# Kernel optimization log

Hardware: AMD Instinct MI355X
Metric: run time of the kernel (lower is better)

## Reference

```python
import jax, jax.numpy as jnp
import numpy as np

N_NODES = 100000


def gcn_layer(x, edge_index, W, b):
    """PyG GCNConv: h = D^-1/2 (A+I) D^-1/2 (x W) + b, scatter-sum aggregation."""
    n = x.shape[0]
    h = x @ W  # [N, out]
    loop = jnp.arange(n, dtype=edge_index.dtype)
    src = jnp.concatenate([edge_index[0], loop])  # [E+N]
    dst = jnp.concatenate([edge_index[1], loop])
    deg = jax.ops.segment_sum(jnp.ones_like(dst, dtype=h.dtype), dst, num_segments=n)
    dinv = jnp.where(deg > 0, jax.lax.rsqrt(deg), 0.0)
    norm = dinv[src] * dinv[dst]  # [E+N]
    msg = h[src] * norm[:, None]  # gather + scale (largest intermediate)
    out = jax.ops.segment_sum(msg, dst, num_segments=n)
    return out + b


def setup_inputs() -> dict:
    key = jax.random.key(0)
    k = jax.random.split(key, 8)
    in_dim, hid_dim, out_dim = 128, 64, 112
    E = 1600000
    x = jax.random.normal(k[0], (N_NODES, in_dim), dtype=jnp.float32)
    edge_index = jax.random.randint(k[1], (2, E), 0, N_NODES, dtype=jnp.int32)
    s1 = 1.0 / np.sqrt(in_dim)
    s2 = 1.0 / np.sqrt(hid_dim)
    return {
        "x": x,
        "edge_index": edge_index,
        "W1": jax.random.uniform(k[2], (in_dim, hid_dim), jnp.float32, -s1, s1),
        "b1": jnp.zeros((hid_dim,), jnp.float32),
        "W2": jax.random.uniform(k[3], (hid_dim, hid_dim), jnp.float32, -s2, s2),
        "b2": jnp.zeros((hid_dim,), jnp.float32),
        "W3": jax.random.uniform(k[4], (hid_dim, out_dim), jnp.float32, -s2, s2),
        "b3": jnp.zeros((out_dim,), jnp.float32),
    }


def reference(x, edge_index, W1, b1, W2, b2, W3, b3):
    # eval mode: dropout is identity
    h = jax.nn.relu(gcn_layer(x, edge_index, W1, b1))
    h = jax.nn.relu(gcn_layer(h, edge_index, W2, b2))
    return gcn_layer(h, edge_index, W3, b3)
```

## Files before the change

### kernel.cpp

```cpp
#include <hip/hip_runtime.h>
#include <hip/hip_fp16.h>
#include <math.h>


#define IN_DIM 128
#define HID 64
#define OUT_DIM 112
#define SCAN_TILE 1024
#define LSHIFT 7
#define LMASK 127
#define MAXBUCK 1024
#define CHUNK 4096
#define CAP 4096

typedef _Float16 f16x8 __attribute__((ext_vector_type(8)));
typedef float f32x4 __attribute__((ext_vector_type(4)));

template <int K, int C, bool XH, bool DINV, bool BIAS, bool OUTH>
__device__ __forceinline__ void mfma_gemm_tile(int blk, const void* __restrict__ Xv,
                                               const float* __restrict__ W,
                                               const float* __restrict__ dinv,
                                               const float* __restrict__ bias,
                                               void* __restrict__ G, int n,
                                               _Float16* Wt) {
  constexpr int KP = K + 8;
  constexpr int NT = C / 16;
  constexpr int KS = K / 32;
  const int tid = threadIdx.x;
  for (int idx = tid; idx < K * C; idx += 256) {
    int k = idx / C, c = idx % C;
    Wt[c * KP + k] = (_Float16)W[idx];
  }
  __syncthreads();

  const int wv = tid >> 6, l = tid & 63;
  const int rbase = blk * 64 + wv * 16;
  const int kg = (l >> 4) * 8;
  const int c16 = l & 15;

  int arow = rbase + c16;
  if (arow >= n) arow = n - 1;
  f16x8 af[KS];
  if (XH) {
    const _Float16* Xh = reinterpret_cast<const _Float16*>(Xv);
#pragma unroll
    for (int ks = 0; ks < KS; ++ks)
      af[ks] = *reinterpret_cast<const f16x8*>(&Xh[(size_t)arow * K + ks * 32 + kg]);
  } else {
    const float* Xf = reinterpret_cast<const float*>(Xv);
#pragma unroll
    for (int ks = 0; ks < KS; ++ks) {
      float4 u0 = *reinterpret_cast<const float4*>(&Xf[(size_t)arow * K + ks * 32 + kg]);
      float4 u1 = *reinterpret_cast<const float4*>(&Xf[(size_t)arow * K + ks * 32 + kg + 4]);
      f16x8 a;
      a[0] = (_Float16)u0.x; a[1] = (_Float16)u0.y; a[2] = (_Float16)u0.z; a[3] = (_Float16)u0.w;
      a[4] = (_Float16)u1.x; a[5] = (_Float16)u1.y; a[6] = (_Float16)u1.z; a[7] = (_Float16)u1.w;
      af[ks] = a;
    }
  }

  f32x4 acc[NT];
#pragma unroll
  for (int nt = 0; nt < NT; ++nt) acc[nt] = (f32x4){0.f, 0.f, 0.f, 0.f};

#pragma unroll
  for (int ks = 0; ks < KS; ++ks) {
#pragma unroll
    for (int nt = 0; nt < NT; ++nt) {
      f16x8 bf = *reinterpret_cast<const f16x8*>(&Wt[(nt * 16 + c16) * KP + ks * 32 + kg]);
      acc[nt] = __builtin_amdgcn_mfma_f32_16x16x32_f16(af[ks], bf, acc[nt], 0, 0, 0);
    }
  }

#pragma unroll
  for (int r = 0; r < 4; ++r) {
    int grow = rbase + (l >> 4) * 4 + r;
    if (grow < n) {
      float s = DINV ? dinv[grow] : 1.0f;
#pragma unroll
      for (int nt = 0; nt < NT; ++nt) {
        float v = acc[nt][r] * s;
        if (BIAS) v += bias[nt * 16 + c16];
        if (OUTH)
          reinterpret_cast<__half*>(G)[(size_t)grow * C + nt * 16 + c16] = __float2half(v);
        else
          reinterpret_cast<float*>(G)[(size_t)grow * C + nt * 16 + c16] = v;
      }
    }
  }
}

template <int K, int C, bool XH, bool DINV, bool BIAS, bool OUTH>
__global__ __launch_bounds__(256) void mfma_gemm_kernel(const void* __restrict__ Xv,
                                                        const float* __restrict__ W,
                                                        const float* __restrict__ dinv,
                                                        const float* __restrict__ bias,
                                                        void* __restrict__ G, int n) {
  __shared__ _Float16 Wt[C * (K + 8)];
  mfma_gemm_tile<K, C, XH, DINV, BIAS, OUTH>(blockIdx.x, Xv, W, dinv, bias, G, n, Wt);
}

__global__ __launch_bounds__(256) void gemm1_scatter_kernel(
    const float* __restrict__ x, const float* __restrict__ W1, __half* __restrict__ gh,
    int n, const int* __restrict__ src, const int* __restrict__ dst,
    int* __restrict__ cur0, int* __restrict__ packed, int E, int nbuck, int nchunk) {
  __shared__ _Float16 Wt[HID * (IN_DIM + 8)];
  __shared__ int hist[MAXBUCK];
  __shared__ int cur[MAXBUCK];
  const int tid = threadIdx.x;
  if ((int)blockIdx.x < nchunk) {
    for (int i = tid; i < nbuck; i += 256) hist[i] = 0;
    __syncthreads();
    const int lo = blockIdx.x * CHUNK;
    const int hi = min(E, lo + CHUNK);
    for (int i = lo + tid; i < hi; i += 256)
      atomicAdd(&hist[dst[i] >> LSHIFT], 1);
    __syncthreads();
    for (int b = tid; b < nbuck; b += 256) {
      int c = hist[b];
      cur[b] = (c > 0) ? atomicAdd(&cur0[b], c) : 0;
    }
    __syncthreads();
    for (int i = lo + tid; i < hi; i += 256) {
      int s = src[i], d = dst[i];
      int b = d >> LSHIFT;
      int off = atomicAdd(&cur[b], 1);
      if (off < CAP) packed[b * CAP + off] = (s << LSHIFT) | (d & LMASK);
    }
  } else {
    mfma_gemm_tile<IN_DIM, HID, false, false, false, true>(
        (int)blockIdx.x - nchunk, x, W1, nullptr, nullptr, gh, n, Wt);
  }
}

__global__ __launch_bounds__(256) void fine_count_kernel(const int* __restrict__ packed,
                                                         const int* __restrict__ cur0,
                                                         int* __restrict__ cnt,
                                                         float* __restrict__ dinv, int n) {
  int b = blockIdx.x;
  __shared__ int hist[128];
  int t = threadIdx.x;
  if (t < 128) hist[t] = 0;
  __syncthreads();
  int cb = min(cur0[b], CAP);
  const int* pk = &packed[b * CAP];
  for (int e = t; e < cb; e += 256) atomicAdd(&hist[pk[e] & LMASK], 1);
  __syncthreads();
  int node = b * 128 + t;
  if (t < 128 && node < n) {
    cnt[node] = hist[t];
    dinv[node] = 1.0f / sqrtf((float)(hist[t] + 1));
  }
}

__global__ __launch_bounds__(256) void fine_scatter_kernel(const int* __restrict__ packed,
                                                           const int* __restrict__ cur0,
                                                           const int* __restrict__ row_start,
                                                           int* __restrict__ ssrc, int n) {
  int b = blockIdx.x;
  __shared__ int cur[128];
  int t = threadIdx.x;
  if (t < 128) {
    int node = b * 128 + t;
    cur[t] = (node < n) ? row_start[node] : 0;
  }
  __syncthreads();
  int cb = min(cur0[b], CAP);
  const int* pk = &packed[b * CAP];
  for (int e = t; e < cb; e += 256) {
    int p = pk[e];
    int slot = atomicAdd(&cur[p & LMASK], 1);
    ssrc[slot] = p >> LSHIFT;
  }
}


__global__ __launch_bounds__(256) void scan_partial_kernel(const int* __restrict__ cnt,
                                                           int* __restrict__ blocksum,
                                                           int n) {
  int t = threadIdx.x;
  int base = blockIdx.x * SCAN_TILE + t * 4;
  int s = 0;
  if (base + 4 <= n) {
    int4 v = *reinterpret_cast<const int4*>(&cnt[base]);
    s = v.x + v.y + v.z + v.w;
  } else {
    for (int i = 0; i < 4; ++i)
      if (base + i < n) s += cnt[base + i];
  }
#pragma unroll
  for (int off = 1; off < 64; off <<= 1) s += __shfl_xor(s, off);
  __shared__ int wsum[4];
  int lane = t & 63, wv = t >> 6;
  if (lane == 0) wsum[wv] = s;
  __syncthreads();
  if (t == 0) blocksum[blockIdx.x] = wsum[0] + wsum[1] + wsum[2] + wsum[3];
}

__global__ __launch_bounds__(1024) void scan_blocksums_kernel(int* __restrict__ blocksum,
                                                              int* __restrict__ total_out,
                                                              int nb) {
  __shared__ int sh[1024];
  int t = threadIdx.x;
  int v = (t < nb) ? blocksum[t] : 0;
  sh[t] = v;
  __syncthreads();
  for (int off = 1; off < 1024; off <<= 1) {
    int u = (t >= off) ? sh[t - off] : 0;
    __syncthreads();
    sh[t] += u;
    __syncthreads();
  }
  if (t < nb) blocksum[t] = sh[t] - v;
  if (t == 1023) *total_out = sh[1023];
}

__global__ __launch_bounds__(256) void scan_final_kernel(const int* __restrict__ cnt,
                                                         const int* __restrict__ blocksum,
                                                         int* __restrict__ row_start, int n) {
  int t = threadIdx.x;
  int base = blockIdx.x * SCAN_TILE + t * 4;
  int v0 = 0, v1 = 0, v2 = 0, v3 = 0;
  if (base + 4 <= n) {
    int4 v = *reinterpret_cast<const int4*>(&cnt[base]);
    v0 = v.x; v1 = v.y; v2 = v.z; v3 = v.w;
  } else {
    if (base + 0 < n) v0 = cnt[base + 0];
    if (base + 1 < n) v1 = cnt[base + 1];
    if (base + 2 < n) v2 = cnt[base + 2];
    if (base + 3 < n) v3 = cnt[base + 3];
  }
  int s = v0 + v1 + v2 + v3;
  __shared__ int sh[256];
  sh[t] = s;
  __syncthreads();
  for (int off = 1; off < 256; off <<= 1) {
    int u = (t >= off) ? sh[t - off] : 0;
    __syncthreads();
    sh[t] += u;
    __syncthreads();
  }
  int run = blocksum[blockIdx.x] + sh[t] - s;
  int p0 = run, p1 = run + v0, p2 = p1 + v1, p3 = p2 + v2;
  if (base + 4 <= n) {
    *reinterpret_cast<int4*>(&row_start[base]) = make_int4(p0, p1, p2, p3);
  } else {
    if (base + 0 < n) row_start[base + 0] = p0;
    if (base + 1 < n) row_start[base + 1] = p1;
    if (base + 2 < n) row_start[base + 2] = p2;
    if (base + 3 < n) row_start[base + 3] = p3;
  }
}

template <int C, bool RELU, bool BIAS, bool TSCALE, bool OUTH, bool SRCSCALE>
__global__ __launch_bounds__(256) void agg_kernel(const __half* __restrict__ g,
                                                  const int* __restrict__ row_start,
                                                  const int* __restrict__ ssrc,
                                                  const float* __restrict__ dinv,
                                                  const float* __restrict__ bias,
                                                  void* __restrict__ out, int n) {
  static_assert(C == 64, "agg assumes 64 channels");
  const int tid = threadIdx.x;
  const int wv = tid >> 6;
  const int lane = tid & 63;
  const int h = lane >> 5;
  const int q = lane & 31;
  int node = blockIdx.x * 4 + wv;
  if (node >= n) return;
  const __half2* g2 = reinterpret_cast<const __half2*>(g);

  int e0 = row_start[node];
  int e1 = row_start[node + 1];
  int deg = e1 - e0;
  float di = dinv[node];
  float2 acc = make_float2(0.f, 0.f);
  if (h == 0) {
    float2 sv = __half22float2(g2[(size_t)node * 32 + q]);
    float w = SRCSCALE ? di : 1.0f;
    acc.x = sv.x * w; acc.y = sv.y * w;
  }
  const int pairs = deg >> 1;
  const int base = e0 + h;
  int k = 0;
  for (; k + 8 <= pairs; k += 8) {
    int idx[8];
#pragma unroll
    for (int i = 0; i < 8; ++i) idx[i] = ssrc[base + 2 * (k + i)];
    __half2 v[8];
#pragma unroll
    for (int i = 0; i < 8; ++i) v[i] = g2[(size_t)idx[i] * 32 + q];
    float ds[8];
    if (SRCSCALE) {
#pragma unroll
      for (int i = 0; i < 8; ++i) ds[i] = dinv[idx[i]];
    }
#pragma unroll
    for (int i = 0; i < 8; ++i) {
      float2 f = __half22float2(v[i]);
      if (SRCSCALE) {
        acc.x = fmaf(f.x, ds[i], acc.x); acc.y = fmaf(f.y, ds[i], acc.y);
      } else {
        acc.x += f.x; acc.y += f.y;
      }
    }
  }
  for (; k < pairs; ++k) {
    int i0 = ssrc[base + 2 * k];
    float2 f = __half22float2(g2[(size_t)i0 * 32 + q]);
    float w = SRCSCALE ? dinv[i0] : 1.0f;
    acc.x = fmaf(f.x, w, acc.x); acc.y = fmaf(f.y, w, acc.y);
  }
  if ((deg & 1) && h == 0) {
    int i0 = ssrc[e1 - 1];
    float2 f = __half22float2(g2[(size_t)i0 * 32 + q]);
    float w = SRCSCALE ? dinv[i0] : 1.0f;
    acc.x = fmaf(f.x, w, acc.x); acc.y = fmaf(f.y, w, acc.y);
  }
  acc.x += __shfl_xor(acc.x, 32);
  acc.y += __shfl_xor(acc.y, 32);

  if (h == 0) {
    float rx = acc.x * di, ry = acc.y * di;
    if (BIAS) {
      float2 bv = *reinterpret_cast<const float2*>(&bias[2 * q]);
      rx += bv.x; ry += bv.y;
    }
    if (RELU) { rx = fmaxf(rx, 0.f); ry = fmaxf(ry, 0.f); }
    if (TSCALE) { rx *= di; ry *= di; }
    if (OUTH) {
      reinterpret_cast<__half2*>(out)[(size_t)node * 32 + q] = __floats2half2_rn(rx, ry);
    } else {
      reinterpret_cast<float2*>(out)[(size_t)node * 32 + q] = make_float2(rx, ry);
    }
  }
}

extern "C" void kernel_launch(void* const* d_in, const int* in_sizes, int n_in,
                              void* d_out, int out_size, void* d_ws, size_t ws_size,
                              hipStream_t stream) {
  const float* x = (const float*)d_in[0];
  const int* ei = (const int*)d_in[1];
  const float* W1 = (const float*)d_in[2];
  const float* b1 = (const float*)d_in[3];
  const float* W2 = (const float*)d_in[4];
  const float* b2 = (const float*)d_in[5];
  const float* W3 = (const float*)d_in[6];
  const float* b3 = (const float*)d_in[7];
  float* out = (float*)d_out;

  const int n = in_sizes[0] / IN_DIM;
  const int E = in_sizes[1] / 2;
  const int* src = ei;
  const int* dst = ei + E;
  const int nbuck = (n + LMASK) >> LSHIFT;
  const int nchunk = (E + CHUNK - 1) / CHUNK;

  char* p = (char*)d_ws;
  auto alloc = [&](size_t bytes) {
    char* q = p;
    p += (bytes + 255) & ~(size_t)255;
    return q;
  };
  float* dinv = (float*)alloc((size_t)n * 4);
  int* row_start = (int*)alloc((size_t)(n + 1) * 4);
  int* cnt = (int*)alloc((size_t)n * 4);
  int* blocksum = (int*)alloc((size_t)1024 * 4);
  int* cur0 = (int*)alloc((size_t)MAXBUCK * 4);
  int* packed = (int*)alloc((size_t)nbuck * CAP * 4);
  int* ssrc = (int*)alloc((size_t)E * 4);
  __half* gh  = (__half*)alloc((size_t)n * HID * 2);
  __half* h1h = (__half*)alloc((size_t)n * HID * 2);
  __half* th  = (__half*)alloc((size_t)n * HID * 2);
  __half* zh  = h1h;

  const int NB = (n + SCAN_TILE - 1) / SCAN_TILE;
  const int GGRID = (n + 63) / 64;

  hipMemsetAsync(cur0, 0, (size_t)nbuck * 4, stream);
  gemm1_scatter_kernel<<<nchunk + GGRID, 256, 0, stream>>>(x, W1, gh, n, src, dst,
                                                           cur0, packed, E, nbuck, nchunk);
  fine_count_kernel<<<nbuck, 256, 0, stream>>>(packed, cur0, cnt, dinv, n);
  scan_partial_kernel<<<NB, 256, 0, stream>>>(cnt, blocksum, n);
  scan_blocksums_kernel<<<1, 1024, 0, stream>>>(blocksum, &row_start[n], NB);
  scan_final_kernel<<<NB, 256, 0, stream>>>(cnt, blocksum, row_start, n);
  fine_scatter_kernel<<<nbuck, 256, 0, stream>>>(packed, cur0, row_start, ssrc, n);

  agg_kernel<HID, true, true, false, true, true><<<(n + 3) / 4, 256, 0, stream>>>(gh, row_start, ssrc, dinv, b1, h1h, n);

  mfma_gemm_kernel<HID, HID, true, true, false, true><<<GGRID, 256, 0, stream>>>(h1h, W2, dinv, nullptr, gh, n);
  agg_kernel<HID, true, true, true, true, false><<<(n + 3) / 4, 256, 0, stream>>>(gh, row_start, ssrc, dinv, b2, th, n);

  agg_kernel<HID, false, false, false, true, false><<<(n + 3) / 4, 256, 0, stream>>>(th, row_start, ssrc, dinv, nullptr, zh, n);
  mfma_gemm_kernel<HID, OUT_DIM, true, false, true, false><<<GGRID, 256, 0, stream>>>(zh, W3, nullptr, b3, out, n);
}
```

Baseline: 384.7 us.

## Fuse fine count, scan, scatter and source prescale into one CSR kernel

Replaces the fine count, three-kernel scan and fine scatter with one per-bucket kernel. Each bucket computes its row offset by summing the coarse bucket counts that precede it, then runs an in-block prefix over its 128 nodes. The same kernel also prescales the layer-1 features by dinv, so the first aggregation no longer gathers dinv for every edge. It additionally merges shared-memory buffers in the first kernel and adds a two-pair unrolled tail loop in aggregation. The cost is a redundant O(nbuck) prefix read per block and an extra read-modify-write pass over the layer-1 feature buffer.

```diff
diff --git a/kernel.cpp b/kernel.cpp
--- a/kernel.cpp
+++ b/kernel.cpp
@@ -6,7 +6,6 @@
 #define IN_DIM 128
 #define HID 64
 #define OUT_DIM 112
-#define SCAN_TILE 1024
 #define LSHIFT 7
 #define LMASK 127
 #define MAXBUCK 1024
@@ -104,11 +103,11 @@
     const float* __restrict__ x, const float* __restrict__ W1, __half* __restrict__ gh,
     int n, const int* __restrict__ src, const int* __restrict__ dst,
     int* __restrict__ cur0, int* __restrict__ packed, int E, int nbuck, int nchunk) {
-  __shared__ _Float16 Wt[HID * (IN_DIM + 8)];
-  __shared__ int hist[MAXBUCK];
-  __shared__ int cur[MAXBUCK];
+  __shared__ __align__(16) char smem[HID * (IN_DIM + 8) * 2];
   const int tid = threadIdx.x;
   if ((int)blockIdx.x < nchunk) {
+    int* hist = reinterpret_cast<int*>(smem);
+    int* cur = hist + MAXBUCK;
     for (int i = tid; i < nbuck; i += 256) hist[i] = 0;
     __syncthreads();
     const int lo = blockIdx.x * CHUNK;
@@ -128,131 +127,80 @@
       if (off < CAP) packed[b * CAP + off] = (s << LSHIFT) | (d & LMASK);
     }
   } else {
+    _Float16* Wt = reinterpret_cast<_Float16*>(smem);
     mfma_gemm_tile<IN_DIM, HID, false, false, false, true>(
         (int)blockIdx.x - nchunk, x, W1, nullptr, nullptr, gh, n, Wt);
   }
 }
 
-__global__ __launch_bounds__(256) void fine_count_kernel(const int* __restrict__ packed,
-                                                         const int* __restrict__ cur0,
-                                                         int* __restrict__ cnt,
-                                                         float* __restrict__ dinv, int n) {
-  int b = blockIdx.x;
+__global__ __launch_bounds__(256) void fine_fused_kernel(
+    const int* __restrict__ packed, const int* __restrict__ cur0,
+    int* __restrict__ row_start, float* __restrict__ dinv,
+    int* __restrict__ ssrc, __half* __restrict__ gh, int n, int nbuck) {
+  const int b = blockIdx.x;
+  const int t = threadIdx.x;
   __shared__ int hist[128];
-  int t = threadIdx.x;
+  __shared__ int pfx[128];
+  __shared__ int cur[128];
+  __shared__ float sdi[128];
+  __shared__ int red[4];
+  __shared__ int sbase;
   if (t < 128) hist[t] = 0;
   __syncthreads();
-  int cb = min(cur0[b], CAP);
-  const int* pk = &packed[b * CAP];
+  const int cb = min(cur0[b], CAP);
+  const int* pk = &packed[(size_t)b * CAP];
   for (int e = t; e < cb; e += 256) atomicAdd(&hist[pk[e] & LMASK], 1);
-  __syncthreads();
-  int node = b * 128 + t;
-  if (t < 128 && node < n) {
-    cnt[node] = hist[t];
-    dinv[node] = 1.0f / sqrtf((float)(hist[t] + 1));
-  }
-}
-
-__global__ __launch_bounds__(256) void fine_scatter_kernel(const int* __restrict__ packed,
-                                                           const int* __restrict__ cur0,
-                                                           const int* __restrict__ row_start,
-                                                           int* __restrict__ ssrc, int n) {
-  int b = blockIdx.x;
-  __shared__ int cur[128];
-  int t = threadIdx.x;
+  int partial = 0;
+  for (int i = t; i < b; i += 256) partial += min(cur0[i], CAP);
+#pragma unroll
+  for (int off = 1; off < 64; off <<= 1) partial += __shfl_xor(partial, off);
+  const int lane = t & 63, wv = t >> 6;
+  if (lane == 0) red[wv] = partial;
+  __syncthreads();
+  if (t == 0) sbase = red[0] + red[1] + red[2] + red[3];
+  if (t < 128) pfx[t] = hist[t];
+  __syncthreads();
+  for (int off = 1; off < 128; off <<= 1) {
+    int u = (t >= off && t < 128) ? pfx[t - off] : 0;
+    __syncthreads();
+    if (t < 128) pfx[t] += u;
+    __syncthreads();
+  }
   if (t < 128) {
     int node = b * 128 + t;
-    cur[t] = (node < n) ? row_start[node] : 0;
-  }
-  __syncthreads();
-  int cb = min(cur0[b], CAP);
-  const int* pk = &packed[b * CAP];
+    if (node < n) {
+      int rs = sbase + pfx[t] - hist[t];
+      row_start[node] = rs;
+      float di = 1.0f / sqrtf((float)(hist[t] + 1));
+      dinv[node] = di;
+      sdi[t] = di;
+      cur[t] = rs;
+    } else {
+      sdi[t] = 0.f;
+      cur[t] = 0;
+    }
+  }
+  if (b == nbuck - 1 && t == 0) row_start[n] = sbase + cb;
+  __syncthreads();
   for (int e = t; e < cb; e += 256) {
     int p = pk[e];
     int slot = atomicAdd(&cur[p & LMASK], 1);
     ssrc[slot] = p >> LSHIFT;
   }
-}
-
-
-__global__ __launch_bounds__(256) void scan_partial_kernel(const int* __restrict__ cnt,
-                                                           int* __restrict__ blocksum,
-                                                           int n) {
-  int t = threadIdx.x;
-  int base = blockIdx.x * SCAN_TILE + t * 4;
-  int s = 0;
-  if (base + 4 <= n) {
-    int4 v = *reinterpret_cast<const int4*>(&cnt[base]);
-    s = v.x + v.y + v.z + v.w;
-  } else {
-    for (int i = 0; i < 4; ++i)
-      if (base + i < n) s += cnt[base + i];
-  }
-#pragma unroll
-  for (int off = 1; off < 64; off <<= 1) s += __shfl_xor(s, off);
-  __shared__ int wsum[4];
-  int lane = t & 63, wv = t >> 6;
-  if (lane == 0) wsum[wv] = s;
-  __syncthreads();
-  if (t == 0) blocksum[blockIdx.x] = wsum[0] + wsum[1] + wsum[2] + wsum[3];
-}
-
-__global__ __launch_bounds__(1024) void scan_blocksums_kernel(int* __restrict__ blocksum,
-                                                              int* __restrict__ total_out,
-                                                              int nb) {
-  __shared__ int sh[1024];
-  int t = threadIdx.x;
-  int v = (t < nb) ? blocksum[t] : 0;
-  sh[t] = v;
-  __syncthreads();
-  for (int off = 1; off < 1024; off <<= 1) {
-    int u = (t >= off) ? sh[t - off] : 0;
-    __syncthreads();
-    sh[t] += u;
-    __syncthreads();
-  }
-  if (t < nb) blocksum[t] = sh[t] - v;
-  if (t == 1023) *total_out = sh[1023];
-}
-
-__global__ __launch_bounds__(256) void scan_final_kernel(const int* __restrict__ cnt,
-                                                         const int* __restrict__ blocksum,
-                                                         int* __restrict__ row_start, int n) {
-  int t = threadIdx.x;
-  int base = blockIdx.x * SCAN_TILE + t * 4;
-  int v0 = 0, v1 = 0, v2 = 0, v3 = 0;
-  if (base + 4 <= n) {
-    int4 v = *reinterpret_cast<const int4*>(&cnt[base]);
-    v0 = v.x; v1 = v.y; v2 = v.z; v3 = v.w;
-  } else {
-    if (base + 0 < n) v0 = cnt[base + 0];
-    if (base + 1 < n) v1 = cnt[base + 1];
-    if (base + 2 < n) v2 = cnt[base + 2];
-    if (base + 3 < n) v3 = cnt[base + 3];
-  }
-  int s = v0 + v1 + v2 + v3;
-  __shared__ int sh[256];
-  sh[t] = s;
-  __syncthreads();
-  for (int off = 1; off < 256; off <<= 1) {
-    int u = (t >= off) ? sh[t - off] : 0;
-    __syncthreads();
-    sh[t] += u;
-    __syncthreads();
-  }
-  int run = blocksum[blockIdx.x] + sh[t] - s;
-  int p0 = run, p1 = run + v0, p2 = p1 + v1, p3 = p2 + v2;
-  if (base + 4 <= n) {
-    *reinterpret_cast<int4*>(&row_start[base]) = make_int4(p0, p1, p2, p3);
-  } else {
-    if (base + 0 < n) row_start[base + 0] = p0;
-    if (base + 1 < n) row_start[base + 1] = p1;
-    if (base + 2 < n) row_start[base + 2] = p2;
-    if (base + 3 < n) row_start[base + 3] = p3;
-  }
-}
-
-template <int C, bool RELU, bool BIAS, bool TSCALE, bool OUTH, bool SRCSCALE>
+  __half2* g2 = reinterpret_cast<__half2*>(gh);
+  for (int i = t; i < 128 * 32; i += 256) {
+    int nd = i >> 5;
+    int node = b * 128 + nd;
+    if (node < n) {
+      int q = i & 31;
+      float2 f = __half22float2(g2[(size_t)node * 32 + q]);
+      float d = sdi[nd];
+      g2[(size_t)node * 32 + q] = __floats2half2_rn(f.x * d, f.y * d);
+    }
+  }
+}
+
+template <int C, bool RELU, bool BIAS, bool TSCALE, bool OUTH>
 __global__ __launch_bounds__(256) void agg_kernel(const __half* __restrict__ g,
                                                   const int* __restrict__ row_start,
                                                   const int* __restrict__ ssrc,
@@ -272,12 +220,10 @@
   int e0 = row_start[node];
   int e1 = row_start[node + 1];
   int deg = e1 - e0;
-  float di = dinv[node];
   float2 acc = make_float2(0.f, 0.f);
   if (h == 0) {
     float2 sv = __half22float2(g2[(size_t)node * 32 + q]);
-    float w = SRCSCALE ? di : 1.0f;
-    acc.x = sv.x * w; acc.y = sv.y * w;
+    acc.x = sv.x; acc.y = sv.y;
   }
   const int pairs = deg >> 1;
   const int base = e0 + h;
@@ -289,37 +235,34 @@
     __half2 v[8];
 #pragma unroll
     for (int i = 0; i < 8; ++i) v[i] = g2[(size_t)idx[i] * 32 + q];
-    float ds[8];
-    if (SRCSCALE) {
-#pragma unroll
-      for (int i = 0; i < 8; ++i) ds[i] = dinv[idx[i]];
-    }
 #pragma unroll
     for (int i = 0; i < 8; ++i) {
       float2 f = __half22float2(v[i]);
-      if (SRCSCALE) {
-        acc.x = fmaf(f.x, ds[i], acc.x); acc.y = fmaf(f.y, ds[i], acc.y);
-      } else {
-        acc.x += f.x; acc.y += f.y;
-      }
-    }
+      acc.x += f.x; acc.y += f.y;
+    }
+  }
+  for (; k + 2 <= pairs; k += 2) {
+    int i0 = ssrc[base + 2 * k];
+    int i1 = ssrc[base + 2 * (k + 1)];
+    float2 f0 = __half22float2(g2[(size_t)i0 * 32 + q]);
+    float2 f1 = __half22float2(g2[(size_t)i1 * 32 + q]);
+    acc.x += f0.x + f1.x; acc.y += f0.y + f1.y;
   }
   for (; k < pairs; ++k) {
     int i0 = ssrc[base + 2 * k];
     float2 f = __half22float2(g2[(size_t)i0 * 32 + q]);
-    float w = SRCSCALE ? dinv[i0] : 1.0f;
-    acc.x = fmaf(f.x, w, acc.x); acc.y = fmaf(f.y, w, acc.y);
+    acc.x += f.x; acc.y += f.y;
   }
   if ((deg & 1) && h == 0) {
     int i0 = ssrc[e1 - 1];
     float2 f = __half22float2(g2[(size_t)i0 * 32 + q]);
-    float w = SRCSCALE ? dinv[i0] : 1.0f;
-    acc.x = fmaf(f.x, w, acc.x); acc.y = fmaf(f.y, w, acc.y);
+    acc.x += f.x; acc.y += f.y;
   }
   acc.x += __shfl_xor(acc.x, 32);
   acc.y += __shfl_xor(acc.y, 32);
 
   if (h == 0) {
+    float di = dinv[node];
     float rx = acc.x * di, ry = acc.y * di;
     if (BIAS) {
       float2 bv = *reinterpret_cast<const float2*>(&bias[2 * q]);
@@ -363,8 +306,6 @@
   };
   float* dinv = (float*)alloc((size_t)n * 4);
   int* row_start = (int*)alloc((size_t)(n + 1) * 4);
-  int* cnt = (int*)alloc((size_t)n * 4);
-  int* blocksum = (int*)alloc((size_t)1024 * 4);
   int* cur0 = (int*)alloc((size_t)MAXBUCK * 4);
   int* packed = (int*)alloc((size_t)nbuck * CAP * 4);
   int* ssrc = (int*)alloc((size_t)E * 4);
@@ -373,23 +314,18 @@
   __half* th  = (__half*)alloc((size_t)n * HID * 2);
   __half* zh  = h1h;
 
-  const int NB = (n + SCAN_TILE - 1) / SCAN_TILE;
   const int GGRID = (n + 63) / 64;
 
-  hipMemsetAsync(cur0, 0, (size_t)nbuck * 4, stream);
+  hipMemsetAsync(cur0, 0, (size_t)MAXBUCK * 4, stream);
   gemm1_scatter_kernel<<<nchunk + GGRID, 256, 0, stream>>>(x, W1, gh, n, src, dst,
                                                            cur0, packed, E, nbuck, nchunk);
-  fine_count_kernel<<<nbuck, 256, 0, stream>>>(packed, cur0, cnt, dinv, n);
-  scan_partial_kernel<<<NB, 256, 0, stream>>>(cnt, blocksum, n);
-  scan_blocksums_kernel<<<1, 1024, 0, stream>>>(blocksum, &row_start[n], NB);
-  scan_final_kernel<<<NB, 256, 0, stream>>>(cnt, blocksum, row_start, n);
-  fine_scatter_kernel<<<nbuck, 256, 0, stream>>>(packed, cur0, row_start, ssrc, n);
-
-  agg_kernel<HID, true, true, false, true, true><<<(n + 3) / 4, 256, 0, stream>>>(gh, row_start, ssrc, dinv, b1, h1h, n);
+  fine_fused_kernel<<<nbuck, 256, 0, stream>>>(packed, cur0, row_start, dinv, ssrc, gh, n, nbuck);
+
+  agg_kernel<HID, true, true, false, true><<<(n + 3) / 4, 256, 0, stream>>>(gh, row_start, ssrc, dinv, b1, h1h, n);
 
   mfma_gemm_kernel<HID, HID, true, true, false, true><<<GGRID, 256, 0, stream>>>(h1h, W2, dinv, nullptr, gh, n);
-  agg_kernel<HID, true, true, true, true, false><<<(n + 3) / 4, 256, 0, stream>>>(gh, row_start, ssrc, dinv, b2, th, n);
-
-  agg_kernel<HID, false, false, false, true, false><<<(n + 3) / 4, 256, 0, stream>>>(th, row_start, ssrc, dinv, nullptr, zh, n);
+  agg_kernel<HID, true, true, true, true><<<(n + 3) / 4, 256, 0, stream>>>(gh, row_start, ssrc, dinv, b2, th, n);
+
+  agg_kernel<HID, false, false, false, true><<<(n + 3) / 4, 256, 0, stream>>>(th, row_start, ssrc, dinv, nullptr, zh, n);
   mfma_gemm_kernel<HID, OUT_DIM, true, false, true, false><<<GGRID, 256, 0, stream>>>(zh, W3, nullptr, b3, out, n);
 }
```

Result: faster. 339.4 us (-11.8%).
